# Kernel optimization log

Hardware: AMD Instinct MI355X
Metric: run time of the kernel (lower is better)

Reference implementation:

```python
import jax, jax.numpy as jnp
import numpy as np

ALPHA = 0.25
GAMMA = 2.0
EPS = 1e-8


def _pairwise_giou_loss(pred, true):
    # pred: (b,1,N,4), true: (b,m,1,4); boxes in [y1,x1,y2,x2] (tfa convention)
    py1, px1, py2, px2 = [pred[..., i] for i in range(4)]
    ty1, tx1, ty2, tx2 = [true[..., i] for i in range(4)]
    p_area = jnp.maximum(py2 - py1, 0.0) * jnp.maximum(px2 - px1, 0.0)
    t_area = jnp.maximum(ty2 - ty1, 0.0) * jnp.maximum(tx2 - tx1, 0.0)
    i_h = jnp.maximum(jnp.minimum(py2, ty2) - jnp.maximum(py1, ty1), 0.0)
    i_w = jnp.maximum(jnp.minimum(px2, tx2) - jnp.maximum(px1, tx1), 0.0)
    inter = i_h * i_w
    union = p_area + t_area - inter
    iou = jnp.where(union > 0, inter / jnp.maximum(union, EPS), 0.0)
    e_h = jnp.maximum(py2, ty2) - jnp.minimum(py1, ty1)
    e_w = jnp.maximum(px2, tx2) - jnp.minimum(px1, tx1)
    enclose = e_h * e_w
    giou = iou - jnp.where(enclose > 0, (enclose - union) / jnp.maximum(enclose, EPS), 0.0)
    return 1.0 - giou  # (b,m,N)


def setup_inputs():
    key = jax.random.key(0)
    k1, k2, k3, k4 = jax.random.split(key, 4)
    b, w, h, c, m = 8, 128, 128, 80, 100
    # probabilities in (0,1) as produced by a sigmoid head
    cls_pred = jax.random.uniform(k1, (b, w, h, c), jnp.float32, 1e-4, 1.0 - 1e-4)
    # raw box coords in grid units (divided by [w,h,w,h] inside the module)
    loc_pred = jax.random.uniform(k2, (b, w, h, 4), jnp.float32) * jnp.asarray([w, h, w, h], jnp.float32)
    labels = jax.random.randint(k3, (b, m), 0, c)
    cls_true = jax.nn.one_hot(labels, c, dtype=jnp.float32)
    loc_true = jax.random.uniform(k4, (b, m, 4), jnp.float32)
    reg_mask = jnp.ones((b, m), jnp.float32)
    return {"cls_pred": cls_pred, "loc_pred": loc_pred, "cls_true": cls_true,
            "loc_true": loc_true, "reg_mask": reg_mask}


def reference(cls_pred, loc_pred, cls_true, loc_true, reg_mask):
    b, w, h, c = cls_pred.shape
    m = cls_true.shape[1]
    cls_true = (cls_true == 1).astype(jnp.float32)
    p = cls_pred.reshape(b, w * h, c)                                      # (b,N,c)
    loc_p = loc_pred.reshape(b, w * h, 4) / jnp.asarray([w, h, w, h], jnp.float32)
    # focal-style pos/neg class costs; contract over c instead of materializing (b,m,N,c)
    neg = (1.0 - ALPHA) * p ** GAMMA * (-jnp.log(1.0 - p + EPS))
    pos = ALPHA * (1.0 - p) ** GAMMA * (-jnp.log(p + EPS))
    cls_loss = jnp.einsum('bnc,bmc->bmn', pos - neg, cls_true)             # (b,m,N)
    reg_loss = jnp.sum(jnp.abs(loc_true[:, :, None, :] - loc_p[:, None, :, :]), axis=-1)
    giou_loss = _pairwise_giou_loss(loc_p[:, None, :, :], loc_true[:, :, None, :])
    total = 2.0 * cls_loss + 5.0 * reg_loss + 2.0 * giou_loss              # (b,m,N)
    argmin_total = jnp.argmin(total, axis=-1).astype(jnp.int32)            # (b,m)
    batch_idx = jnp.broadcast_to(jnp.arange(b, dtype=jnp.int32)[:, None], (b, m))
    cls_id = jnp.argmax(cls_true, axis=-1).astype(jnp.int32)
    return jnp.stack([batch_idx, argmin_total, cls_id], axis=-1)           # (b,m,3) int32
```

## Files before the change

kernel.cpp:

```cpp
#include <hip/hip_runtime.h>
#include <stdint.h>

#define B    8
#define C    80
#define M    100
#define NPIX 16384
#define NT   32
#define KT   2
#define BT   128
#define NW   4

#define ALPHA_F 0.25f
#define EPS_F   1e-8f

#define SWZ(c) ((((c) & 31)) ^ ((((c) >> 5)) << 3))

__device__ __forceinline__ uint32_t fkey(float f) {
    uint32_t u = __float_as_uint(f);
    return (u & 0x80000000u) ? ~u : (u | 0x80000000u);
}

__global__ __launch_bounds__(256) void init_kernel(
    const float* __restrict__ cls_true,
    int* __restrict__ cids,
    unsigned long long* __restrict__ keys)
{
    const int bm   = blockIdx.x * NW + (threadIdx.x >> 6);
    const int lane = threadIdx.x & 63;
    if (bm >= B * M) return;

    const float* ct = cls_true + (size_t)bm * C;
    const float v0 = ct[lane];
    unsigned long long k =
        ((unsigned long long)fkey(v0) << 32) | (unsigned int)(C - 1 - lane);
    if (lane + 64 < C) {
        const float v1 = ct[lane + 64];
        unsigned long long k1 =
            ((unsigned long long)fkey(v1) << 32) | (unsigned int)(C - 1 - (lane + 64));
        if (k1 > k) k = k1;
    }
    #pragma unroll
    for (int off = 32; off > 0; off >>= 1) {
        unsigned long long o = __shfl_xor(k, off, 64);
        if (o > k) k = o;
    }
    if (lane == 0) {
        cids[bm] = C - 1 - (int)(k & 0xFFFFFFFFull);
        keys[bm] = 0xFFFFFFFFFFFFFFFFull;
    }
}

__global__ __launch_bounds__(256) void prep_kernel(
    const float* __restrict__ loc_pred,
    float* __restrict__ pbox)
{
#pragma clang fp contract(off)
    const int i = blockIdx.x * 256 + threadIdx.x;
    if (i >= B * NPIX) return;
    const float inv = 1.0f / 128.0f;
    const float4 lp = ((const float4*)loc_pred)[i];
    const float py1 = lp.x * inv;
    const float px1 = lp.y * inv;
    const float py2 = lp.z * inv;
    const float px2 = lp.w * inv;
    const float pa  = fmaxf(py2 - py1, 0.0f) * fmaxf(px2 - px1, 0.0f);
    float4* dst = (float4*)pbox + (size_t)i * 2;
    dst[0] = make_float4(py1, px1, py2, px2);
    dst[1] = make_float4(pa, 0.0f, 0.0f, 0.0f);
}

__global__ __launch_bounds__(BT) void match_kernel(
    const float* __restrict__ cls_pred,
    const float* __restrict__ pbox,
    const float* __restrict__ loc_true,
    const int*   __restrict__ cids,
    unsigned long long* __restrict__ keys)
{
#pragma clang fp contract(off)
    __shared__ float D[2][C * NT];

    const int b      = blockIdx.y;
    const int base_n = blockIdx.x * (NT * KT);
    const int tid    = threadIdx.x;
    const int lane   = tid & 63;
    const int w      = tid >> 6;

    const int  mm  = w * 64 + lane;
    const bool act = (mm < M);
    const int  bm  = b * M + (act ? mm : 0);
    int cid = 0, drow = 0, sw = 0;
    float ty1 = 0.f, tx1 = 0.f, ty2 = 0.f, tx2 = 0.f, t_area = 0.f;
    if (act) {
        cid = cids[bm];
        const float4 lt = *(const float4*)(loc_true + (size_t)bm * 4);
        ty1 = lt.x; tx1 = lt.y; ty2 = lt.z; tx2 = lt.w;
        t_area = fmaxf(ty2 - ty1, 0.0f) * fmaxf(tx2 - tx1, 0.0f);
        drow = cid * NT;
        sw   = SWZ(cid) & (NT - 1);
    }

    {
        const float4* src4 = (const float4*)(cls_pred + ((size_t)b * NPIX + base_n) * C);
        #pragma unroll
        for (int it = 0; it < NT * C / 4 / BT; ++it) {
            const int idx4 = it * BT + tid;
            const int n    = idx4 / 20;
            const int c0   = (idx4 - n * 20) * 4;
            const float4 v = src4[idx4];
            const float pv[4] = { v.x, v.y, v.z, v.w };
            #pragma unroll
            for (int jj = 0; jj < 4; ++jj) {
                const int c = c0 + jj;
                const float p = pv[jj];
                const float q = 1.0f - p;
                const float pos = (ALPHA_F * (q * q)) * (-logf(p + EPS_F));
                const float neg = ((1.0f - ALPHA_F) * (p * p)) * (-logf(q + EPS_F));
                D[0][c * NT + ((n ^ SWZ(c)) & (NT - 1))] = pos - neg;
            }
        }
    }
    __syncthreads();

    float bestv = __builtin_huge_valf();
    int   bestn = 0;

    #pragma unroll
    for (int t = 0; t < KT; ++t) {
        const int cur = t & 1;
        const int tn0 = base_n + t * NT;

        float4 ld[5];
        if (t + 1 < KT) {
            const float4* src4 =
                (const float4*)(cls_pred + ((size_t)b * NPIX + tn0 + NT) * C);
            #pragma unroll
            for (int it = 0; it < 5; ++it) ld[it] = src4[it * BT + tid];
        }

        if (act) {
            const float* pb = pbox + ((size_t)(b * NPIX) + tn0) * 8;
            #pragma unroll 8
            for (int j = 0; j < NT; ++j) {
                const float d   = D[cur][drow + (j ^ sw)];
                const float py1 = pb[j * 8 + 0];
                const float px1 = pb[j * 8 + 1];
                const float py2 = pb[j * 8 + 2];
                const float px2 = pb[j * 8 + 3];
                const float pa  = pb[j * 8 + 4];

                const float r = ((fabsf(ty1 - py1) + fabsf(tx1 - px1))
                                 + fabsf(ty2 - py2)) + fabsf(tx2 - px2);

                const float ih = fmaxf(fminf(py2, ty2) - fmaxf(py1, ty1), 0.0f);
                const float iw = fmaxf(fminf(px2, tx2) - fmaxf(px1, tx1), 0.0f);
                const float inter = ih * iw;
                const float uni   = (pa + t_area) - inter;
                const float iou   = (uni > 0.0f) ? (inter / fmaxf(uni, EPS_F)) : 0.0f;
                const float eh = fmaxf(py2, ty2) - fminf(py1, ty1);
                const float ew = fmaxf(px2, tx2) - fminf(px1, tx1);
                const float enc = eh * ew;
                const float pen = (enc > 0.0f) ? ((enc - uni) / fmaxf(enc, EPS_F)) : 0.0f;
                const float gl  = 1.0f - (iou - pen);

                const float total = ((2.0f * d) + (5.0f * r)) + (2.0f * gl);

                if (total < bestv) { bestv = total; bestn = tn0 + j; }
            }
        }

        if (t + 1 < KT) {
            #pragma unroll
            for (int it = 0; it < 5; ++it) {
                const int idx4 = it * BT + tid;
                const int n    = idx4 / 20;
                const int c0   = (idx4 - n * 20) * 4;
                const float pv[4] = { ld[it].x, ld[it].y, ld[it].z, ld[it].w };
                #pragma unroll
                for (int jj = 0; jj < 4; ++jj) {
                    const int c = c0 + jj;
                    const float p = pv[jj];
                    const float q = 1.0f - p;
                    const float pos = (ALPHA_F * (q * q)) * (-logf(p + EPS_F));
                    const float neg = ((1.0f - ALPHA_F) * (p * p)) * (-logf(q + EPS_F));
                    D[1 - cur][c * NT + ((n ^ SWZ(c)) & (NT - 1))] = pos - neg;
                }
            }
            __syncthreads();
        }
    }

    if (act) {
        const unsigned long long key =
            ((unsigned long long)fkey(bestv) << 32) | (unsigned int)bestn;
        atomicMin(&keys[bm], key);
    }
}

__global__ void write_out_kernel(const unsigned long long* __restrict__ keys,
                                 const int* __restrict__ cids,
                                 int* __restrict__ out) {
    int i = blockIdx.x * blockDim.x + threadIdx.x;
    if (i >= B * M) return;
    out[i * 3 + 0] = i / M;
    out[i * 3 + 1] = (int)(keys[i] & 0xFFFFFFFFull);
    out[i * 3 + 2] = cids[i];
}

extern "C" void kernel_launch(void* const* d_in, const int* in_sizes, int n_in,
                              void* d_out, int out_size, void* d_ws, size_t ws_size,
                              hipStream_t stream) {
    const float* cls_pred = (const float*)d_in[0];
    const float* loc_pred = (const float*)d_in[1];
    const float* cls_true = (const float*)d_in[2];
    const float* loc_true = (const float*)d_in[3];
    int* out = (int*)d_out;

    unsigned long long* keys = (unsigned long long*)d_ws;
    int*   cids = (int*)((char*)d_ws + (size_t)B * M * sizeof(unsigned long long));
    float* pbox = (float*)((char*)d_ws + 16384);

    init_kernel<<<(B * M + NW - 1) / NW, 256, 0, stream>>>(cls_true, cids, keys);
    prep_kernel<<<(B * NPIX + 255) / 256, 256, 0, stream>>>(loc_pred, pbox);
    match_kernel<<<dim3(NPIX / (NT * KT), B), BT, 0, stream>>>(
        cls_pred, pbox, loc_true, cids, keys);
    write_out_kernel<<<(B * M + 255) / 256, 256, 0, stream>>>(keys, cids, out);
}
```

Baseline: 60.33 us.

## Use fast log/divide intrinsics with top-2 gap certification and exact fallback

Replaces logf and IEEE divides in the matching kernel with __logf and __fdividef to cut transcendental and division cost. To keep the argmin exact, each thread also tracks the runner-up cost, a second key array merges it across blocks, and rows whose top-two gap is below a small threshold are flagged. A new exact kernel recomputes the full argmin with precise math for flagged rows. This adds an extra launch and extra atomics, and the certification margin may not cover every approximation error.

```diff
diff --git a/kernel.cpp b/kernel.cpp
--- a/kernel.cpp
+++ b/kernel.cpp
@@ -10,8 +10,9 @@
 #define BT   128
 #define NW   4
 
-#define ALPHA_F 0.25f
-#define EPS_F   1e-8f
+#define ALPHA_F  0.25f
+#define EPS_F    1e-8f
+#define CERT_GAP 1e-4f
 
 #define SWZ(c) ((((c) & 31)) ^ ((((c) >> 5)) << 3))
 
@@ -19,11 +20,15 @@
     uint32_t u = __float_as_uint(f);
     return (u & 0x80000000u) ? ~u : (u | 0x80000000u);
 }
+__device__ __forceinline__ float unfkey(uint32_t k) {
+    return __uint_as_float((k & 0x80000000u) ? (k & 0x7FFFFFFFu) : ~k);
+}
 
 __global__ __launch_bounds__(256) void init_kernel(
     const float* __restrict__ cls_true,
     int* __restrict__ cids,
-    unsigned long long* __restrict__ keys)
+    unsigned long long* __restrict__ keys,
+    unsigned long long* __restrict__ keys2)
 {
     const int bm   = blockIdx.x * NW + (threadIdx.x >> 6);
     const int lane = threadIdx.x & 63;
@@ -45,8 +50,9 @@
         if (o > k) k = o;
     }
     if (lane == 0) {
-        cids[bm] = C - 1 - (int)(k & 0xFFFFFFFFull);
-        keys[bm] = 0xFFFFFFFFFFFFFFFFull;
+        cids[bm]  = C - 1 - (int)(k & 0xFFFFFFFFull);
+        keys[bm]  = 0xFFFFFFFFFFFFFFFFull;
+        keys2[bm] = 0xFFFFFFFFFFFFFFFFull;
     }
 }
 
@@ -74,7 +80,8 @@
     const float* __restrict__ pbox,
     const float* __restrict__ loc_true,
     const int*   __restrict__ cids,
-    unsigned long long* __restrict__ keys)
+    unsigned long long* __restrict__ keys,
+    unsigned long long* __restrict__ keys2)
 {
 #pragma clang fp contract(off)
     __shared__ float D[2][C * NT];
@@ -113,16 +120,17 @@
                 const int c = c0 + jj;
                 const float p = pv[jj];
                 const float q = 1.0f - p;
-                const float pos = (ALPHA_F * (q * q)) * (-logf(p + EPS_F));
-                const float neg = ((1.0f - ALPHA_F) * (p * p)) * (-logf(q + EPS_F));
+                const float pos = (ALPHA_F * (q * q)) * (-__logf(p + EPS_F));
+                const float neg = ((1.0f - ALPHA_F) * (p * p)) * (-__logf(q + EPS_F));
                 D[0][c * NT + ((n ^ SWZ(c)) & (NT - 1))] = pos - neg;
             }
         }
     }
     __syncthreads();
 
-    float bestv = __builtin_huge_valf();
-    int   bestn = 0;
+    float b1v = __builtin_huge_valf();
+    float b2v = __builtin_huge_valf();
+    int   b1n = 0;
 
     #pragma unroll
     for (int t = 0; t < KT; ++t) {
@@ -155,16 +163,19 @@
                 const float iw = fmaxf(fminf(px2, tx2) - fmaxf(px1, tx1), 0.0f);
                 const float inter = ih * iw;
                 const float uni   = (pa + t_area) - inter;
-                const float iou   = (uni > 0.0f) ? (inter / fmaxf(uni, EPS_F)) : 0.0f;
+                const float iou   = (uni > 0.0f)
+                    ? __fdividef(inter, fmaxf(uni, EPS_F)) : 0.0f;
                 const float eh = fmaxf(py2, ty2) - fminf(py1, ty1);
                 const float ew = fmaxf(px2, tx2) - fminf(px1, tx1);
                 const float enc = eh * ew;
-                const float pen = (enc > 0.0f) ? ((enc - uni) / fmaxf(enc, EPS_F)) : 0.0f;
+                const float pen = (enc > 0.0f)
+                    ? __fdividef(enc - uni, fmaxf(enc, EPS_F)) : 0.0f;
                 const float gl  = 1.0f - (iou - pen);
 
                 const float total = ((2.0f * d) + (5.0f * r)) + (2.0f * gl);
 
-                if (total < bestv) { bestv = total; bestn = tn0 + j; }
+                if (total < b1v)      { b2v = b1v; b1v = total; b1n = tn0 + j; }
+                else if (total < b2v) { b2v = total; }
             }
         }
 
@@ -180,8 +191,8 @@
                     const int c = c0 + jj;
                     const float p = pv[jj];
                     const float q = 1.0f - p;
-                    const float pos = (ALPHA_F * (q * q)) * (-logf(p + EPS_F));
-                    const float neg = ((1.0f - ALPHA_F) * (p * p)) * (-logf(q + EPS_F));
+                    const float pos = (ALPHA_F * (q * q)) * (-__logf(p + EPS_F));
+                    const float neg = ((1.0f - ALPHA_F) * (p * p)) * (-__logf(q + EPS_F));
                     D[1 - cur][c * NT + ((n ^ SWZ(c)) & (NT - 1))] = pos - neg;
                 }
             }
@@ -190,20 +201,109 @@
     }
 
     if (act) {
-        const unsigned long long key =
-            ((unsigned long long)fkey(bestv) << 32) | (unsigned int)bestn;
-        atomicMin(&keys[bm], key);
+        const unsigned long long k1 =
+            ((unsigned long long)fkey(b1v) << 32) | (unsigned int)b1n;
+        const unsigned long long k2 = ((unsigned long long)fkey(b2v) << 32);
+
+        const unsigned long long cur1 = keys[bm];
+        unsigned long long loser = k1;
+        if (k1 < cur1) {
+            const unsigned long long old = atomicMin(&keys[bm], k1);
+            loser = (k1 < old) ? old : k1;
+        }
+        const unsigned long long cand2 = (loser < k2) ? loser : k2;
+        const unsigned long long cur2  = keys2[bm];
+        if (cand2 < cur2) atomicMin(&keys2[bm], cand2);
     }
 }
 
 __global__ void write_out_kernel(const unsigned long long* __restrict__ keys,
+                                 const unsigned long long* __restrict__ keys2,
                                  const int* __restrict__ cids,
-                                 int* __restrict__ out) {
+                                 int* __restrict__ out,
+                                 int* __restrict__ flags) {
     int i = blockIdx.x * blockDim.x + threadIdx.x;
     if (i >= B * M) return;
     out[i * 3 + 0] = i / M;
     out[i * 3 + 1] = (int)(keys[i] & 0xFFFFFFFFull);
     out[i * 3 + 2] = cids[i];
+    const float v1 = unfkey((uint32_t)(keys[i] >> 32));
+    const float v2 = unfkey((uint32_t)(keys2[i] >> 32));
+    flags[i] = (v2 - v1 <= CERT_GAP) ? 1 : 0;
+}
+
+__global__ __launch_bounds__(1024) void exact_fix_kernel(
+    const float* __restrict__ cls_pred,
+    const float* __restrict__ loc_pred,
+    const float* __restrict__ loc_true,
+    const int*   __restrict__ cids,
+    const int*   __restrict__ flags,
+    int* __restrict__ out)
+{
+#pragma clang fp contract(off)
+    const int bm = blockIdx.x;
+    if (!flags[bm]) return;
+
+    const int b   = bm / M;
+    const int tid = threadIdx.x;
+    const int cid = cids[bm];
+
+    const float4 lt = *(const float4*)(loc_true + (size_t)bm * 4);
+    const float ty1 = lt.x, tx1 = lt.y, ty2 = lt.z, tx2 = lt.w;
+    const float t_area = fmaxf(ty2 - ty1, 0.0f) * fmaxf(tx2 - tx1, 0.0f);
+    const float inv = 1.0f / 128.0f;
+
+    unsigned long long best = 0xFFFFFFFFFFFFFFFFull;
+
+    for (int n = tid; n < NPIX; n += 1024) {
+        const float p = cls_pred[((size_t)b * NPIX + n) * C + cid];
+        const float q = 1.0f - p;
+        const float pos = (ALPHA_F * (q * q)) * (-logf(p + EPS_F));
+        const float neg = ((1.0f - ALPHA_F) * (p * p)) * (-logf(q + EPS_F));
+        const float d   = pos - neg;
+
+        const float4 lp = *(const float4*)(loc_pred + ((size_t)b * NPIX + n) * 4);
+        const float py1 = lp.x * inv;
+        const float px1 = lp.y * inv;
+        const float py2 = lp.z * inv;
+        const float px2 = lp.w * inv;
+        const float pa  = fmaxf(py2 - py1, 0.0f) * fmaxf(px2 - px1, 0.0f);
+
+        const float r = ((fabsf(ty1 - py1) + fabsf(tx1 - px1))
+                         + fabsf(ty2 - py2)) + fabsf(tx2 - px2);
+
+        const float ih = fmaxf(fminf(py2, ty2) - fmaxf(py1, ty1), 0.0f);
+        const float iw = fmaxf(fminf(px2, tx2) - fmaxf(px1, tx1), 0.0f);
+        const float inter = ih * iw;
+        const float uni   = (pa + t_area) - inter;
+        const float iou   = (uni > 0.0f) ? (inter / fmaxf(uni, EPS_F)) : 0.0f;
+        const float eh = fmaxf(py2, ty2) - fminf(py1, ty1);
+        const float ew = fmaxf(px2, tx2) - fminf(px1, tx1);
+        const float enc = eh * ew;
+        const float pen = (enc > 0.0f) ? ((enc - uni) / fmaxf(enc, EPS_F)) : 0.0f;
+        const float gl  = 1.0f - (iou - pen);
+
+        const float total = ((2.0f * d) + (5.0f * r)) + (2.0f * gl);
+
+        const unsigned long long key =
+            ((unsigned long long)fkey(total) << 32) | (unsigned int)n;
+        if (key < best) best = key;
+    }
+
+    #pragma unroll
+    for (int off = 32; off > 0; off >>= 1) {
+        unsigned long long o = __shfl_xor(best, off, 64);
+        if (o < best) best = o;
+    }
+    __shared__ unsigned long long red[16];
+    if ((tid & 63) == 0) red[tid >> 6] = best;
+    __syncthreads();
+    if (tid == 0) {
+        unsigned long long r = red[0];
+        #pragma unroll
+        for (int i = 1; i < 16; ++i) if (red[i] < r) r = red[i];
+        out[bm * 3 + 1] = (int)(r & 0xFFFFFFFFull);
+    }
 }
 
 extern "C" void kernel_launch(void* const* d_in, const int* in_sizes, int n_in,
@@ -215,13 +315,17 @@
     const float* loc_true = (const float*)d_in[3];
     int* out = (int*)d_out;
 
-    unsigned long long* keys = (unsigned long long*)d_ws;
-    int*   cids = (int*)((char*)d_ws + (size_t)B * M * sizeof(unsigned long long));
-    float* pbox = (float*)((char*)d_ws + 16384);
-
-    init_kernel<<<(B * M + NW - 1) / NW, 256, 0, stream>>>(cls_true, cids, keys);
+    unsigned long long* keys  = (unsigned long long*)d_ws;
+    unsigned long long* keys2 = (unsigned long long*)((char*)d_ws + 6400);
+    int*   cids  = (int*)((char*)d_ws + 12800);
+    int*   flags = (int*)((char*)d_ws + 16000);
+    float* pbox  = (float*)((char*)d_ws + 32768);
+
+    init_kernel<<<(B * M + NW - 1) / NW, 256, 0, stream>>>(cls_true, cids, keys, keys2);
     prep_kernel<<<(B * NPIX + 255) / 256, 256, 0, stream>>>(loc_pred, pbox);
     match_kernel<<<dim3(NPIX / (NT * KT), B), BT, 0, stream>>>(
-        cls_pred, pbox, loc_true, cids, keys);
-    write_out_kernel<<<(B * M + 255) / 256, 256, 0, stream>>>(keys, cids, out);
-}
+        cls_pred, pbox, loc_true, cids, keys, keys2);
+    write_out_kernel<<<(B * M + 255) / 256, 256, 0, stream>>>(keys, keys2, cids, out, flags);
+    exact_fix_kernel<<<B * M, 1024, 0, stream>>>(
+        cls_pred, loc_pred, loc_true, cids, flags, out);
+}
```

Measured after the change: 78.58 us. 30.2% more time.
